# Kernel optimization log

Measured on AMD Instinct MI355X. Metric: run time of the kernel, lower is better.

Reference implementation:

```python
import jax, jax.numpy as jnp
import numpy as np

N = 50000       # nodes per subgraph scale
E = 800000      # edges per subgraph scale
B = 4096        # number of subgraphs (graphs in the batch)
IN, HID, OUT = 64, 64, 32
NE = 8          # num_experts
EMB = 64        # emb_dim per expert
E2 = 131072     # graph-level edges for distortion loss


def setup_inputs() -> dict:
    key = jax.random.key(0)
    ks = jax.random.split(key, 16)
    inv = lambda d: 1.0 / np.sqrt(d)
    return {
        "subgraph_x0": jax.random.normal(ks[0], (N, IN), jnp.float32),
        "subgraph_x1": jax.random.normal(ks[1], (N, IN), jnp.float32),
        "W1": jax.random.normal(ks[2], (IN, HID), jnp.float32) * inv(IN),
        "b1": jnp.zeros((HID,), jnp.float32),
        "W2": jax.random.normal(ks[3], (HID, OUT), jnp.float32) * inv(HID),
        "b2": jnp.zeros((OUT,), jnp.float32),
        "Wc": jax.random.normal(ks[4], (OUT * 2, NE), jnp.float32) * inv(OUT * 2),
        "bc": jnp.zeros((NE,), jnp.float32),
        "embeddings": jax.random.normal(ks[5], (B, NE * EMB), jnp.float32),
        # precomputed shortest-path distances per graph edge (positive)
        "dis": jax.random.uniform(ks[6], (E2,), jnp.float32) * 1.5 + 0.5,
        "edge_index0": jax.random.randint(ks[7], (2, E), 0, N, jnp.int32),
        "edge_index1": jax.random.randint(ks[8], (2, E), 0, N, jnp.int32),
        "batch0": jnp.sort(jax.random.randint(ks[9], (N,), 0, B, jnp.int32)),
        "batch1": jnp.sort(jax.random.randint(ks[10], (N,), 0, B, jnp.int32)),
        "edge_index2": jax.random.randint(ks[11], (2, E2), 0, B, jnp.int32),
        "emb_dim": EMB,
    }


def _gcn_conv(x, W, b, src, dst, n):
    """PyG GCNConv: D^{-1/2}(A+I)D^{-1/2} X W + b, with self-loops."""
    xw = x @ W  # [n, out]
    ones = jnp.ones(src.shape, xw.dtype)
    deg = jax.ops.segment_sum(ones, dst, num_segments=n) + 1.0  # self-loop degree
    dinv = jax.lax.rsqrt(deg)  # [n]
    norm = dinv[src] * dinv[dst]  # [E]
    agg = jax.ops.segment_sum(xw[src] * norm[:, None], dst, num_segments=n)
    agg = agg + (dinv * dinv)[:, None] * xw  # self-loop messages
    return agg + b


def _mean_pool(x, batch, num_graphs):
    s = jax.ops.segment_sum(x, batch, num_segments=num_graphs)
    cnt = jax.ops.segment_sum(jnp.ones((x.shape[0],), x.dtype), batch,
                              num_segments=num_graphs)
    return s / jnp.maximum(cnt, 1.0)[:, None]


def _encode_scale(x, edge_index, batch, W1, b1, W2, b2, num_graphs):
    src, dst = edge_index[0], edge_index[1]
    n = x.shape[0]
    h = _gcn_conv(x, W1, b1, src, dst, n)
    h = _gcn_conv(h, W2, b2, src, dst, n)
    return _mean_pool(h, batch, num_graphs)


def reference(subgraph_x0, subgraph_x1, W1, b1, W2, b2, Wc, bc,
              embeddings, dis, edge_index0, edge_index1,
              batch0, batch1, edge_index2, emb_dim):
    num_graphs = embeddings.shape[0]
    x0 = _encode_scale(subgraph_x0, edge_index0, batch0, W1, b1, W2, b2, num_graphs)
    x1 = _encode_scale(subgraph_x1, edge_index1, batch1, W1, b1, W2, b2, num_graphs)
    x = jnp.concatenate([x0, x1], axis=-1)  # [B, 2*OUT]
    gate = jax.nn.softmax(x @ Wc + bc, axis=-1)  # temperature = 1.0

    # distortion loss over graph-level edges
    s, d = edge_index2[0], edge_index2[1]
    e = edge_index2.shape[1]
    diff = (embeddings[s] - embeddings[d]) ** 2  # [E2, NE*emb_dim]
    diff = diff.reshape(e, diff.shape[1] // emb_dim, emb_dim).sum(axis=2)  # [E2, NE]
    weights = jax.nn.softmax(gate[s] * gate[d], axis=1)  # [E2, NE]
    dsum = jnp.sum(diff * weights, axis=-1)  # [E2]
    loss_distortion = jnp.mean(jnp.abs(dsum / dis - 1.0))
    return gate, loss_distortion
```

## Files before the change

### kernel.cpp

```cpp
#include <hip/hip_runtime.h>
#include <math.h>

constexpr int IN_F  = 64;
constexpr int HID_F = 64;
constexpr int OUT_F = 32;
constexpr int NEXP  = 8;
constexpr int EMB   = 64;


__device__ __forceinline__ unsigned short f2b(float x) {
    unsigned u = __float_as_uint(x);
    unsigned r = (u + 0x7FFFu + ((u >> 16) & 1u)) >> 16;
    return (unsigned short)r;
}
__device__ __forceinline__ float b2f(unsigned short h) {
    return __uint_as_float(((unsigned)h) << 16);
}

__global__ void zero_f32_kernel(float* __restrict__ p, long long n) {
    long long i = (long long)blockIdx.x * blockDim.x + threadIdx.x;
    long long stride = (long long)gridDim.x * blockDim.x;
    for (; i < n; i += stride) p[i] = 0.0f;
}

__global__ void zero_i32_kernel(int* __restrict__ p, long long n) {
    long long i = (long long)blockIdx.x * blockDim.x + threadIdx.x;
    long long stride = (long long)gridDim.x * blockDim.x;
    for (; i < n; i += stride) p[i] = 0;
}

__global__ __launch_bounds__(1024)
void w12_kernel(const float* __restrict__ W1, const float* __restrict__ W2,
                const float* __restrict__ b1,
                float* __restrict__ W12, float* __restrict__ c1)
{
    __shared__ float sW2[HID_F * OUT_F];
    const int tid = threadIdx.x;
    for (int i = tid; i < HID_F * OUT_F; i += 1024) sW2[i] = W2[i];
    __syncthreads();
    for (int idx = tid; idx < IN_F * OUT_F; idx += 1024) {
        int i = idx >> 5, j = idx & 31;
        float acc = 0.0f;
#pragma unroll
        for (int k = 0; k < HID_F; ++k) acc += W1[i * HID_F + k] * sW2[k * OUT_F + j];
        W12[idx] = acc;
    }
    if (tid < OUT_F) {
        float acc = 0.0f;
#pragma unroll
        for (int k = 0; k < HID_F; ++k) acc += b1[k] * sW2[k * OUT_F + tid];
        c1[tid] = acc;
    }
}

__global__ void hist2_kernel(const int* __restrict__ ei0, const int* __restrict__ ei1,
                             int* __restrict__ counts, int E, int N)
{
    int e = blockIdx.x * blockDim.x + threadIdx.x;
    if (e >= 2 * E) return;
    int d = (e < E) ? ei0[E + e] : (ei1[E + (e - E)] + N);
    atomicAdd(&counts[d], 1);
}

__global__ __launch_bounds__(1024)
void scan1_kernel(const int* __restrict__ counts, int* __restrict__ lexcl,
                  int* __restrict__ partials, int N)
{
    __shared__ int wsum[16];
    const int tid  = threadIdx.x;
    const int lane = tid & 63;
    const int wv   = tid >> 6;
    const int i    = blockIdx.x * 1024 + tid;

    int v = (i < N) ? counts[i] : 0;
    int x = v;
#pragma unroll
    for (int off = 1; off < 64; off <<= 1) {
        int t = __shfl_up(x, off);
        if (lane >= off) x += t;
    }
    if (lane == 63) wsum[wv] = x;
    __syncthreads();
    int woff = 0;
    for (int w = 0; w < wv; ++w) woff += wsum[w];
    if (i < N) lexcl[i] = woff + x - v;
    if (tid == 1023) partials[blockIdx.x] = woff + x;
}

__global__ __launch_bounds__(1024)
void scan2_kernel(int* __restrict__ partials, int NB)
{
    __shared__ int wsum[16];
    const int tid  = threadIdx.x;
    const int lane = tid & 63;
    const int wv   = tid >> 6;
    int v = (tid < NB) ? partials[tid] : 0;
    int x = v;
#pragma unroll
    for (int off = 1; off < 64; off <<= 1) {
        int t = __shfl_up(x, off);
        if (lane >= off) x += t;
    }
    if (lane == 63) wsum[wv] = x;
    __syncthreads();
    int woff = 0;
    for (int w = 0; w < wv; ++w) woff += wsum[w];
    if (tid < NB) partials[tid] = woff + x - v;
}

__global__ void scan3_kernel(const int* __restrict__ lexcl, const int* __restrict__ partials,
                             const int* __restrict__ counts,
                             int* __restrict__ offsets, int* __restrict__ cursor,
                             float* __restrict__ dinv, int n2, int e2tot)
{
    int i = blockIdx.x * blockDim.x + threadIdx.x;
    if (i >= n2) return;
    int o = lexcl[i] + partials[i >> 10];
    offsets[i] = o;
    cursor[i]  = o;
    dinv[i] = rsqrtf((float)counts[i] + 1.0f);
    if (i == 0) offsets[n2] = e2tot;
}

__global__ __launch_bounds__(256)
void scatter2_shard_kernel(const int* __restrict__ ei0, const int* __restrict__ ei1,
                           int* __restrict__ cursor, int* __restrict__ csr_src,
                           int E, int N, int n2)
{
    const int shard   = blockIdx.x & 7;
    const int bid     = blockIdx.x >> 3;
    const int nblocks = gridDim.x >> 3;
    const int lo = (int)(((long long)n2 * shard) >> 3);
    const int hi = (int)(((long long)n2 * (shard + 1)) >> 3);

    long long start  = (long long)bid * blockDim.x + threadIdx.x;
    long long stride = (long long)nblocks * blockDim.x;
    const long long e2 = 2LL * E;
    for (long long e = start; e < e2; e += stride) {
        int s, d;
        if (e < E) { s = ei0[e];                 d = ei0[E + e]; }
        else       { s = ei1[e - E] + N;         d = ei1[E + (e - E)] + N; }
        if (d >= lo && d < hi) {
            int pos = atomicAdd(&cursor[d], 1);
            csr_src[pos] = s;
        }
    }
}

__global__ __launch_bounds__(256)
void gemm_ys2_kernel(const float* __restrict__ x0, const float* __restrict__ x1,
                     const float* __restrict__ W12, const float* __restrict__ dinv,
                     unsigned short* __restrict__ Ysh, int N, int n2)
{
    __shared__ float Ws[IN_F * OUT_F];
    __shared__ float xs[8 * IN_F];
    const int tid = threadIdx.x;

    for (int i = tid; i < IN_F * OUT_F; i += 256) Ws[i] = W12[i];
    const int row0 = blockIdx.x * 8;
    for (int i = tid; i < 8 * IN_F; i += 256) {
        int r = i >> 6;
        int rr = row0 + r;
        float v = 0.0f;
        if (rr < n2) {
            v = (rr < N) ? x0[(size_t)rr * IN_F + (i & 63)]
                         : x1[(size_t)(rr - N) * IN_F + (i & 63)];
        }
        xs[i] = v;
    }
    __syncthreads();

    const int r = tid >> 5;
    const int c = tid & 31;
    const int row = row0 + r;
    if (row >= n2) return;

    float acc = 0.0f;
#pragma unroll
    for (int k = 0; k < IN_F; ++k) acc += xs[r * IN_F + k] * Ws[k * OUT_F + c];

    Ysh[(size_t)row * OUT_F + c] = f2b(acc * dinv[row]);
}

template<int MODE>
__global__ __launch_bounds__(256)
void csr_agg32_kernel(const int* __restrict__ csr_src, const int* __restrict__ offsets,
                      const unsigned short* __restrict__ in, const float* __restrict__ dinv,
                      float* __restrict__ sdsum, const float* __restrict__ c1,
                      const float* __restrict__ b2,
                      unsigned short* __restrict__ outh, float* __restrict__ outf, int n)
{
    constexpr int F = OUT_F;
    const int lane = threadIdx.x & 63;
    const int wid  = (blockIdx.x * (blockDim.x >> 6)) + (threadIdx.x >> 6);
    const int sub  = lane >> 5;
    const int f    = lane & 31;
    const int node = wid * 2 + sub;
    const int lbase = sub * F;

    const bool valid = (node < n);
    const int nc   = valid ? node : 0;
    const int off0 = offsets[nc];
    const int off1 = valid ? offsets[nc + 1] : off0;

    float acc0 = valid ? b2f(in[(size_t)nc * F + f]) : 0.0f;
    float acc1 = 0.0f, acc2 = 0.0f, acc3 = 0.0f;
    float dsum = 0.0f;
    for (int k = off0; k < off1; k += F) {
        int nk = off1 - k; if (nk > F) nk = F;
        int sj = (f < nk) ? csr_src[k + f] : 0;
        if (MODE == 0) {
            float dv = dinv[sj];
            dsum += (f < nk) ? dv : 0.0f;
        }
        int t = 0;
        for (; t + 8 <= nk; t += 8) {
            int s0 = __shfl(sj, lbase + t);
            int s1 = __shfl(sj, lbase + t + 1);
            int s2 = __shfl(sj, lbase + t + 2);
            int s3 = __shfl(sj, lbase + t + 3);
            int s4 = __shfl(sj, lbase + t + 4);
            int s5 = __shfl(sj, lbase + t + 5);
            int s6 = __shfl(sj, lbase + t + 6);
            int s7 = __shfl(sj, lbase + t + 7);
            float v0 = b2f(in[(size_t)s0 * F + f]);
            float v1 = b2f(in[(size_t)s1 * F + f]);
            float v2 = b2f(in[(size_t)s2 * F + f]);
            float v3 = b2f(in[(size_t)s3 * F + f]);
            float v4 = b2f(in[(size_t)s4 * F + f]);
            float v5 = b2f(in[(size_t)s5 * F + f]);
            float v6 = b2f(in[(size_t)s6 * F + f]);
            float v7 = b2f(in[(size_t)s7 * F + f]);
            acc0 += v0 + v4;
            acc1 += v1 + v5;
            acc2 += v2 + v6;
            acc3 += v3 + v7;
        }
        for (; t < nk; ++t) {
            int s = __shfl(sj, lbase + t);
            acc0 += b2f(in[(size_t)s * F + f]);
        }
    }
    if (MODE == 0) {
#pragma unroll
        for (int off = 1; off < 32; off <<= 1) dsum += __shfl_xor(dsum, off);
    }
    if (valid) {
        float di = dinv[node];
        float s = (acc0 + acc1) + (acc2 + acc3);
        if (MODE == 0) {
            outh[(size_t)node * F + f] = f2b(di * di * s);
            if (f == 0) sdsum[node] = dsum;
        } else {
            float t = di * (di + sdsum[node]);
            outf[(size_t)node * F + f] = di * s + t * c1[f] + b2[f];
        }
    }
}

__global__ void pool_sum2_kernel(const float* __restrict__ h,
                                 const int* __restrict__ bat0, const int* __restrict__ bat1,
                                 float* __restrict__ pooled, float* __restrict__ cnt,
                                 int N, int n2, int B)
{
    int t = blockIdx.x * blockDim.x + threadIdx.x;
    int i = t >> 5;
    int f = t & 31;
    if (i >= n2) return;
    int g = (i < N) ? bat0[i] : (bat1[i - N] + B);
    atomicAdd(&pooled[(size_t)g * OUT_F + f], h[(size_t)i * OUT_F + f]);
    if (f == 0) atomicAdd(&cnt[g], 1.0f);
}

__global__ void gate_kernel(const float* __restrict__ pooled, const float* __restrict__ cnt,
                            const float* __restrict__ Wc, const float* __restrict__ bc,
                            float* __restrict__ gate, float* __restrict__ loss_out, int B)
{
    int g = blockIdx.x * blockDim.x + threadIdx.x;
    if (g == 0) *loss_out = 0.0f;
    if (g >= B) return;
    float inv0 = 1.0f / fmaxf(cnt[g], 1.0f);
    float inv1 = 1.0f / fmaxf(cnt[B + g], 1.0f);
    float xv[2 * OUT_F];
#pragma unroll
    for (int k = 0; k < OUT_F; ++k) xv[k] = pooled[(size_t)g * OUT_F + k] * inv0;
#pragma unroll
    for (int k = 0; k < OUT_F; ++k)
        xv[OUT_F + k] = pooled[(size_t)(B + g) * OUT_F + k] * inv1;

    float lg[NEXP];
    float m = -1e30f;
#pragma unroll
    for (int e = 0; e < NEXP; ++e) {
        float acc = bc[e];
#pragma unroll
        for (int k = 0; k < 2 * OUT_F; ++k) acc += xv[k] * Wc[k * NEXP + e];
        lg[e] = acc;
        m = fmaxf(m, acc);
    }
    float se = 0.0f;
#pragma unroll
    for (int e = 0; e < NEXP; ++e) { lg[e] = expf(lg[e] - m); se += lg[e]; }
    float inv = 1.0f / se;
#pragma unroll
    for (int e = 0; e < NEXP; ++e) gate[(size_t)g * NEXP + e] = lg[e] * inv;
}

__global__ void histK_kernel(const int* __restrict__ s_idx, const int* __restrict__ d_idx,
                             int* __restrict__ histK, int E2, int B, int quarter)
{
    int e = blockIdx.x * blockDim.x + threadIdx.x;
    if (e >= E2) return;
    int qd = d_idx[e] / quarter; if (qd > 3) qd = 3;
    atomicAdd(&histK[qd * B + s_idx[e]], 1);
}

__global__ void combineK_kernel(const int* __restrict__ lexclK, const int* __restrict__ partialsK,
                                int* __restrict__ offK, int* __restrict__ curK, int nk, int E2)
{
    int i = blockIdx.x * blockDim.x + threadIdx.x;
    if (i >= nk) return;
    int o = lexclK[i] + partialsK[i >> 10];
    offK[i] = o;
    curK[i] = o;
    if (i == 0) offK[nk] = E2;
}

__global__ void scatterK_kernel(const int* __restrict__ s_idx, const int* __restrict__ d_idx,
                                const float* __restrict__ dis,
                                int* __restrict__ curK, int* __restrict__ dD,
                                float* __restrict__ disD, int E2, int B, int quarter)
{
    int e = blockIdx.x * blockDim.x + threadIdx.x;
    if (e >= E2) return;
    int d = d_idx[e];
    int qd = d / quarter; if (qd > 3) qd = 3;
    int pos = atomicAdd(&curK[qd * B + s_idx[e]], 1);
    dD[pos] = d;
    disD[pos] = dis[e];
}

__global__ __launch_bounds__(256)
void distortion6_kernel(const float* __restrict__ emb, const float* __restrict__ gate,
                        const int* __restrict__ offK, const int* __restrict__ dD,
                        const float* __restrict__ disD,
                        float* __restrict__ loss, int B, int E2)
{
    const int lane = threadIdx.x & 63;
    const int q    = lane >> 4;
    const int ql   = lane & 15;
    const int xcd  = blockIdx.x & 7;
    const int bid  = blockIdx.x >> 3;
    const int wv   = threadIdx.x >> 6;
    const int wIdx = bid * 4 + wv;
    const int nws  = (gridDim.x >> 3) * 4;

    const int qd   = xcd >> 1;
    const int sh   = xcd & 1;
    const int halfB = B >> 1;
    const int k0 = qd * B + sh * halfB;
    const int k1 = qd * B + (sh ? B : halfB);

    const float4* emb4  = (const float4*)emb;
    const float4* gate4 = (const float4*)gate;

    float lsum = 0.0f;
    for (int k = k0 + wIdx; k < k1; k += nws) {
        const int j0 = offK[k];
        const int j1 = offK[k + 1];
        if (j0 == j1) continue;
        const int s = k - qd * B;

        const float4* es = emb4 + (size_t)s * 128;
        float4 a0 = es[ql];
        float4 a1 = es[ql + 16];
        float4 a2 = es[ql + 32];
        float4 a3 = es[ql + 48];
        float4 a4 = es[ql + 64];
        float4 a5 = es[ql + 80];
        float4 a6 = es[ql + 96];
        float4 a7 = es[ql + 112];
        float4 gs0 = gate4[(size_t)s * 2];
        float4 gs1 = gate4[(size_t)s * 2 + 1];

        for (int j = j0 + q; j < j1; j += 4) {
            int d = dD[j];
            float dv = disD[j];
            const float4* ed = emb4 + (size_t)d * 128;
            float4 b0 = ed[ql];
            float4 b1 = ed[ql + 16];
            float4 b2 = ed[ql + 32];
            float4 b3 = ed[ql + 48];
            float4 b4 = ed[ql + 64];
            float4 b5 = ed[ql + 80];
            float4 b6 = ed[ql + 96];
            float4 b7 = ed[ql + 112];
            float4 gd0 = gate4[(size_t)d * 2];
            float4 gd1 = gate4[(size_t)d * 2 + 1];

            float p[NEXP];
            float dx;
            dx = a0.x - b0.x; p[0]  = dx * dx;
            dx = a0.y - b0.y; p[0] += dx * dx;
            dx = a0.z - b0.z; p[0] += dx * dx;
            dx = a0.w - b0.w; p[0] += dx * dx;
            dx = a1.x - b1.x; p[1]  = dx * dx;
            dx = a1.y - b1.y; p[1] += dx * dx;
            dx = a1.z - b1.z; p[1] += dx * dx;
            dx = a1.w - b1.w; p[1] += dx * dx;
            dx = a2.x - b2.x; p[2]  = dx * dx;
            dx = a2.y - b2.y; p[2] += dx * dx;
            dx = a2.z - b2.z; p[2] += dx * dx;
            dx = a2.w - b2.w; p[2] += dx * dx;
            dx = a3.x - b3.x; p[3]  = dx * dx;
            dx = a3.y - b3.y; p[3] += dx * dx;
            dx = a3.z - b3.z; p[3] += dx * dx;
            dx = a3.w - b3.w; p[3] += dx * dx;
            dx = a4.x - b4.x; p[4]  = dx * dx;
            dx = a4.y - b4.y; p[4] += dx * dx;
            dx = a4.z - b4.z; p[4] += dx * dx;
            dx = a4.w - b4.w; p[4] += dx * dx;
            dx = a5.x - b5.x; p[5]  = dx * dx;
            dx = a5.y - b5.y; p[5] += dx * dx;
            dx = a5.z - b5.z; p[5] += dx * dx;
            dx = a5.w - b5.w; p[5] += dx * dx;
            dx = a6.x - b6.x; p[6]  = dx * dx;
            dx = a6.y - b6.y; p[6] += dx * dx;
            dx = a6.z - b6.z; p[6] += dx * dx;
            dx = a6.w - b6.w; p[6] += dx * dx;
            dx = a7.x - b7.x; p[7]  = dx * dx;
            dx = a7.y - b7.y; p[7] += dx * dx;
            dx = a7.z - b7.z; p[7] += dx * dx;
            dx = a7.w - b7.w; p[7] += dx * dx;

#pragma unroll
            for (int off = 1; off < 16; off <<= 1) {
#pragma unroll
                for (int t = 0; t < NEXP; ++t) p[t] += __shfl_xor(p[t], off);
            }

            float gp[NEXP] = { gs0.x * gd0.x, gs0.y * gd0.y, gs0.z * gd0.z, gs0.w * gd0.w,
                               gs1.x * gd1.x, gs1.y * gd1.y, gs1.z * gd1.z, gs1.w * gd1.w };
            float m = gp[0];
#pragma unroll
            for (int t = 1; t < NEXP; ++t) m = fmaxf(m, gp[t]);
            float se = 0.0f;
#pragma unroll
            for (int t = 0; t < NEXP; ++t) { gp[t] = expf(gp[t] - m); se += gp[t]; }
            float dsum = 0.0f;
#pragma unroll
            for (int t = 0; t < NEXP; ++t) dsum += p[t] * gp[t];

            lsum += fabsf((dsum / se) / dv - 1.0f);
        }
    }
    lsum += __shfl_xor(lsum, 16);
    lsum += __shfl_xor(lsum, 32);
    if (lane == 0) atomicAdd(loss, lsum / (float)E2);
}

extern "C" void kernel_launch(void* const* d_in, const int* in_sizes, int n_in,
                              void* d_out, int out_size, void* d_ws, size_t ws_size,
                              hipStream_t stream)
{
    const float* x0   = (const float*)d_in[0];
    const float* x1   = (const float*)d_in[1];
    const float* W1   = (const float*)d_in[2];
    const float* b1   = (const float*)d_in[3];
    const float* W2   = (const float*)d_in[4];
    const float* b2   = (const float*)d_in[5];
    const float* Wc   = (const float*)d_in[6];
    const float* bc   = (const float*)d_in[7];
    const float* emb  = (const float*)d_in[8];
    const float* dis  = (const float*)d_in[9];
    const int*   ei0  = (const int*)d_in[10];
    const int*   ei1  = (const int*)d_in[11];
    const int*   bat0 = (const int*)d_in[12];
    const int*   bat1 = (const int*)d_in[13];
    const int*   ei2  = (const int*)d_in[14];

    const int N  = in_sizes[0] / IN_F;
    const int E  = in_sizes[10] / 2;
    const int B  = in_sizes[8] / (NEXP * EMB);
    const int E2 = in_sizes[14] / 2;
    const int n2 = 2 * N;
    const int nk = 4 * B;
    const int quarter = (B + 3) / 4;

    float* gate_out = (float*)d_out;
    float* loss_out = gate_out + (size_t)B * NEXP;

    float* ws      = (float*)d_ws;
    float* dinv    = ws;
    float* Ys      = dinv + n2;
    float* Zs      = Ys + (size_t)n2 * OUT_F;
    float* sdsum   = Zs + (size_t)n2 * OUT_F;
    float* pooled  = sdsum + n2;
    float* cnt     = pooled + (size_t)2 * B * OUT_F;
    float* W12     = cnt + 2 * B;
    float* c1      = W12 + IN_F * OUT_F;
    float* disD    = c1 + OUT_F;
    int*   iws     = (int*)(disD + E2);
    int*   counts  = iws;
    int*   histK   = counts + n2;
    int*   offsets = histK + nk;
    int*   cursor  = offsets + n2 + 1;
    int*   csr_src = cursor + n2;
    int*   lexcl   = csr_src + 2 * E;
    int*   partials= lexcl + n2;
    int*   lexclK  = partials + 1024;
    int*   partialsK = lexclK + nk;
    int*   offK    = partialsK + 1024;
    int*   curK    = offK + nk + 1;
    int*   dD      = curK + nk;

    unsigned short* Ysh = (unsigned short*)Ys;
    unsigned short* Zsh = (unsigned short*)Zs;
    float* P = Ys;

    const int TB = 256;
    const int zgrid = 512;
    const int NB2 = (n2 + 1023) / 1024;
    const int NBK = (nk + 1023) / 1024;

    w12_kernel<<<1, 1024, 0, stream>>>(W1, W2, b1, W12, c1);

    zero_i32_kernel<<<zgrid, TB, 0, stream>>>(counts, (long long)n2 + nk);
    hist2_kernel<<<(2 * E + TB - 1) / TB, TB, 0, stream>>>(ei0, ei1, counts, E, N);
    scan1_kernel<<<NB2, 1024, 0, stream>>>(counts, lexcl, partials, n2);
    scan2_kernel<<<1, 1024, 0, stream>>>(partials, NB2);
    scan3_kernel<<<(n2 + TB - 1) / TB, TB, 0, stream>>>(lexcl, partials, counts,
                                                        offsets, cursor, dinv, n2, 2 * E);
    scatter2_shard_kernel<<<1024, TB, 0, stream>>>(ei0, ei1, cursor, csr_src, E, N, n2);

    histK_kernel<<<(E2 + TB - 1) / TB, TB, 0, stream>>>(ei2, ei2 + E2, histK, E2, B, quarter);
    scan1_kernel<<<NBK, 1024, 0, stream>>>(histK, lexclK, partialsK, nk);
    scan2_kernel<<<1, 1024, 0, stream>>>(partialsK, NBK);
    combineK_kernel<<<(nk + TB - 1) / TB, TB, 0, stream>>>(lexclK, partialsK, offK, curK, nk, E2);
    scatterK_kernel<<<(E2 + TB - 1) / TB, TB, 0, stream>>>(ei2, ei2 + E2, dis,
                                                           curK, dD, disD, E2, B, quarter);

    gemm_ys2_kernel<<<(n2 + 7) / 8, 256, 0, stream>>>(x0, x1, W12, dinv, Ysh, N, n2);
    csr_agg32_kernel<0><<<(n2 + 7) / 8, TB, 0, stream>>>(csr_src, offsets, Ysh, dinv,
                                                         sdsum, nullptr, nullptr,
                                                         Zsh, nullptr, n2);
    csr_agg32_kernel<1><<<(n2 + 7) / 8, TB, 0, stream>>>(csr_src, offsets, Zsh, dinv,
                                                         sdsum, c1, b2,
                                                         nullptr, P, n2);

    zero_f32_kernel<<<zgrid, TB, 0, stream>>>(pooled, (long long)2 * B * OUT_F + 2 * B);
    pool_sum2_kernel<<<((n2 * 32) + TB - 1) / TB, TB, 0, stream>>>(P, bat0, bat1,
                                                                   pooled, cnt, N, n2, B);

    gate_kernel<<<(B + TB - 1) / TB, TB, 0, stream>>>(pooled, cnt, Wc, bc,
                                                      gate_out, loss_out, B);

    distortion6_kernel<<<1024, TB, 0, stream>>>(emb, gate_out, offK, dD, disD,
                                                loss_out, B, E2);
}
```

Baseline: 393.2 us.

## Build CSR via two-pass bucketed scatter through 16-node buckets

Replaces the single-pass scatter of edge sources into CSR with two passes. The first pass scatters (dst, src) pairs into coarse buckets of 16 destination nodes using per-bucket cursors. The second pass streams that bucket buffer and does the final per-node atomic placement. The aim is to make the final scatter's writes and atomics local to nearby memory instead of random across the whole array. In exchange it adds an extra pass, twice the bytes per edge in the intermediate buffer, and reuses the Ys workspace for that buffer, so Ys must be large enough (2*n2*OUT_F floats covers 2E int2) and written only afterwards.

```diff
diff --git a/kernel.cpp b/kernel.cpp
--- a/kernel.cpp
+++ b/kernel.cpp
@@ -111,6 +111,7 @@
 __global__ void scan3_kernel(const int* __restrict__ lexcl, const int* __restrict__ partials,
                              const int* __restrict__ counts,
                              int* __restrict__ offsets, int* __restrict__ cursor,
+                             int* __restrict__ cursor64,
                              float* __restrict__ dinv, int n2, int e2tot)
 {
     int i = blockIdx.x * blockDim.x + threadIdx.x;
@@ -118,20 +119,21 @@
     int o = lexcl[i] + partials[i >> 10];
     offsets[i] = o;
     cursor[i]  = o;
+    if ((i & 15) == 0) cursor64[i >> 4] = o;
     dinv[i] = rsqrtf((float)counts[i] + 1.0f);
     if (i == 0) offsets[n2] = e2tot;
 }
 
 __global__ __launch_bounds__(256)
-void scatter2_shard_kernel(const int* __restrict__ ei0, const int* __restrict__ ei1,
-                           int* __restrict__ cursor, int* __restrict__ csr_src,
-                           int E, int N, int n2)
+void bucket_scatter_kernel(const int* __restrict__ ei0, const int* __restrict__ ei1,
+                           int* __restrict__ cursor64, int2* __restrict__ bucketBuf,
+                           int E, int N, int nbuck)
 {
     const int shard   = blockIdx.x & 7;
     const int bid     = blockIdx.x >> 3;
     const int nblocks = gridDim.x >> 3;
-    const int lo = (int)(((long long)n2 * shard) >> 3);
-    const int hi = (int)(((long long)n2 * (shard + 1)) >> 3);
+    const int blo = (int)(((long long)nbuck * shard) >> 3);
+    const int bhi = (int)(((long long)nbuck * (shard + 1)) >> 3);
 
     long long start  = (long long)bid * blockDim.x + threadIdx.x;
     long long stride = (long long)nblocks * blockDim.x;
@@ -140,11 +142,23 @@
         int s, d;
         if (e < E) { s = ei0[e];                 d = ei0[E + e]; }
         else       { s = ei1[e - E] + N;         d = ei1[E + (e - E)] + N; }
-        if (d >= lo && d < hi) {
-            int pos = atomicAdd(&cursor[d], 1);
-            csr_src[pos] = s;
-        }
-    }
+        int b = d >> 4;
+        if (b >= blo && b < bhi) {
+            int pos = atomicAdd(&cursor64[b], 1);
+            bucketBuf[pos] = make_int2(d, s);
+        }
+    }
+}
+
+__global__ __launch_bounds__(256)
+void csr_fill_kernel(const int2* __restrict__ bucketBuf, int* __restrict__ cursor,
+                     int* __restrict__ csr_src, long long e2)
+{
+    long long i = (long long)blockIdx.x * blockDim.x + threadIdx.x;
+    if (i >= e2) return;
+    int2 ed = bucketBuf[i];
+    int pos = atomicAdd(&cursor[ed.x], 1);
+    csr_src[pos] = ed.y;
 }
 
 __global__ __launch_bounds__(256)
@@ -486,6 +500,7 @@
     const int n2 = 2 * N;
     const int nk = 4 * B;
     const int quarter = (B + 3) / 4;
+    const int nbuck = (n2 + 15) / 16;
 
     float* gate_out = (float*)d_out;
     float* loss_out = gate_out + (size_t)B * NEXP;
@@ -513,9 +528,11 @@
     int*   offK    = partialsK + 1024;
     int*   curK    = offK + nk + 1;
     int*   dD      = curK + nk;
+    int*   cursor64= dD + E2;
 
     unsigned short* Ysh = (unsigned short*)Ys;
     unsigned short* Zsh = (unsigned short*)Zs;
+    int2* bucketBuf = (int2*)Ys;
     float* P = Ys;
 
     const int TB = 256;
@@ -530,8 +547,11 @@
     scan1_kernel<<<NB2, 1024, 0, stream>>>(counts, lexcl, partials, n2);
     scan2_kernel<<<1, 1024, 0, stream>>>(partials, NB2);
     scan3_kernel<<<(n2 + TB - 1) / TB, TB, 0, stream>>>(lexcl, partials, counts,
-                                                        offsets, cursor, dinv, n2, 2 * E);
-    scatter2_shard_kernel<<<1024, TB, 0, stream>>>(ei0, ei1, cursor, csr_src, E, N, n2);
+                                                        offsets, cursor, cursor64,
+                                                        dinv, n2, 2 * E);
+    bucket_scatter_kernel<<<1024, TB, 0, stream>>>(ei0, ei1, cursor64, bucketBuf, E, N, nbuck);
+    csr_fill_kernel<<<(int)((2LL * E + TB - 1) / TB), TB, 0, stream>>>(bucketBuf, cursor,
+                                                                       csr_src, 2LL * E);
 
     histK_kernel<<<(E2 + TB - 1) / TB, TB, 0, stream>>>(ei2, ei2 + E2, histK, E2, B, quarter);
     scan1_kernel<<<NBK, 1024, 0, stream>>>(histK, lexclK, partialsK, nk);
```

Result: slower. 509.2 us (+29.5%).
